# Performance work log

Hardware: AMD Instinct MI355X
Metric: run time of the kernel (lower is better)

The kernel has to match this reference:

```python
import jax, jax.numpy as jnp
import numpy as np

NUM_NODES = 100000
EMBED_DIM = 64
NUM_EDGES = 1250000
NUM_LAYERS = 3


def setup_inputs() -> dict:
    key = jax.random.key(0)
    k1, k2 = jax.random.split(key)
    edge_index = jax.random.randint(k1, (2, NUM_EDGES), 0, NUM_NODES, dtype=jnp.int32)
    # nn.init.normal_(std=0.1)
    emb = 0.1 * jax.random.normal(k2, (NUM_NODES, EMBED_DIM), dtype=jnp.float32)
    return {"edge_index": edge_index, "emb": emb}


def reference(edge_index, emb):
    n = emb.shape[0]
    row, col = edge_index[0], edge_index[1]  # row = source j, col = target i
    # degree of target nodes (PyG degree(col, N))
    deg = jax.ops.segment_sum(jnp.ones((row.shape[0],), emb.dtype), col, num_segments=n)
    deg_inv_sqrt = jnp.where(deg > 0, jax.lax.rsqrt(jnp.maximum(deg, 1.0)), 0.0).astype(emb.dtype)
    norm = deg_inv_sqrt[row] * deg_inv_sqrt[col]  # [E]

    x = emb
    acc = emb  # running sum over layer embeddings (layer 0 included)
    for _ in range(NUM_LAYERS):
        # gather-scale-scatter: out[i] = sum_{(j->i)} norm * x[j]
        msgs = norm[:, None] * x[row]                       # [E, d]
        x = jax.ops.segment_sum(msgs, col, num_segments=n)  # [N, d]
        acc = acc + x
    return acc / (NUM_LAYERS + 1)
```

## Files before the change

kernel.cpp:

```cpp
#include <hip/hip_runtime.h>


#define BKT_SHIFT 7
#define BKT_NODES 128
#define BKT_CAP   2560
#define EPB       2048

__device__ __forceinline__ float lo2f(unsigned u) { return __uint_as_float(u << 16); }
__device__ __forceinline__ float hi2f(unsigned u) { return __uint_as_float(u & 0xFFFF0000u); }
__device__ __forceinline__ unsigned cvt_pk_bf16(float lo, float hi) {
  unsigned r;
  asm("v_cvt_pk_bf16_f32 %0, %1, %2" : "=v"(r) : "v"(lo), "v"(hi));
  return r;
}

__device__ __forceinline__ int wave_scan_incl(int v, int lane) {
#pragma unroll
  for (int off = 1; off < 64; off <<= 1) {
    int t = __shfl_up(v, off, 64);
    if (lane >= off) v += t;
  }
  return v;
}

__global__ void k_init(int* __restrict__ bcursor, int nbkt,
                       unsigned* __restrict__ z0, unsigned* __restrict__ z1,
                       unsigned* __restrict__ z2, int n) {
  int i = blockIdx.x * blockDim.x + threadIdx.x;
  if (i < nbkt) bcursor[i] = i * BKT_CAP;
  if (blockIdx.x == 0 && threadIdx.x < 32) {
    size_t o = (size_t)n * 32 + threadIdx.x;
    z0[o] = 0u; z1[o] = 0u; z2[o] = 0u;
  }
}

__global__ __launch_bounds__(256)
void k_bin(const int* __restrict__ row, const int* __restrict__ col,
           int* __restrict__ bcursor, int* __restrict__ tmp, int E, int nbkt) {
  __shared__ int h[1024];
  int e0 = blockIdx.x * EPB;
  int e1 = min(e0 + EPB, E);
  for (int i = threadIdx.x; i < nbkt; i += 256) h[i] = 0;
  __syncthreads();
  for (int e = e0 + threadIdx.x; e < e1; e += 256)
    atomicAdd(&h[col[e] >> BKT_SHIFT], 1);
  __syncthreads();
  for (int i = threadIdx.x; i < nbkt; i += 256) {
    int c = h[i];
    h[i] = c ? atomicAdd(&bcursor[i], c) : 0;
  }
  __syncthreads();
  for (int e = e0 + threadIdx.x; e < e1; e += 256) {
    int c = col[e], r = row[e];
    int p = atomicAdd(&h[c >> BKT_SHIFT], 1);
    tmp[p] = r | ((c & (BKT_NODES - 1)) << 20);
  }
}

__global__ __launch_bounds__(256)
void k_sort(const int* __restrict__ bcursor, const int* __restrict__ tmp,
            int* __restrict__ srcs, int* __restrict__ obeg, int* __restrict__ oend,
            float* __restrict__ invdeg, float* __restrict__ sdeg,
            const float* __restrict__ emb, unsigned short* __restrict__ z0, int n) {
  __shared__ int hist[BKT_NODES];
  __shared__ int excl[BKT_NODES];
  __shared__ int cur[BKT_NODES];
  __shared__ float sdis[BKT_NODES];
  int b = blockIdx.x;
  int base = b * BKT_CAP;
  int cnt = bcursor[b] - base;
  if (threadIdx.x < BKT_NODES) hist[threadIdx.x] = 0;
  __syncthreads();
  for (int q = threadIdx.x; q < cnt; q += 256)
    atomicAdd(&hist[(unsigned)tmp[base + q] >> 20], 1);
  __syncthreads();
  if (threadIdx.x < 64) {
    int l = threadIdx.x;
    int h0 = hist[2 * l], h1 = hist[2 * l + 1];
    int p0 = (h0 + 3) & ~3, p1 = (h1 + 3) & ~3;
    int v = p0 + p1;
    int incl = wave_scan_incl(v, l);
    int ex = incl - v;
    excl[2 * l] = ex;      excl[2 * l + 1] = ex + p0;
    cur[2 * l] = ex;       cur[2 * l + 1] = ex + p0;
  }
  __syncthreads();
  int node0 = b << BKT_SHIFT;
  if (threadIdx.x < BKT_NODES) {
    int node = node0 + threadIdx.x;
    if (node < n) {
      int d = hist[threadIdx.x];
      int dpad = (d + 3) & ~3;
      int bg = base + excl[threadIdx.x];
      obeg[node] = bg;
      oend[node] = bg + dpad;
      float fd = (float)d;
      invdeg[node] = d ? 1.0f / fd : 0.0f;
      sdeg[node] = sqrtf(fd);
      sdis[threadIdx.x] = d ? rsqrtf(fd) : 0.0f;
      for (int p = d; p < dpad; ++p) srcs[bg + p] = n;
    } else {
      sdis[threadIdx.x] = 0.0f;
    }
  }
  __syncthreads();
  for (int q = threadIdx.x; q < cnt; q += 256) {
    int rec = tmp[base + q];
    int lc = (unsigned)rec >> 20;
    int p = atomicAdd(&cur[lc], 1);
    srcs[base + p] = rec & 0xFFFFF;
  }
  int nloc = min(BKT_NODES, n - node0);
  for (int t = threadIdx.x; t < nloc * 8; t += 256) {
    int rr = t >> 3, q = t & 7;
    float ds = sdis[rr];
    float4 v0 = reinterpret_cast<const float4*>(emb)[(size_t)(node0 + rr) * 16 + 2 * q];
    float4 v1 = reinterpret_cast<const float4*>(emb)[(size_t)(node0 + rr) * 16 + 2 * q + 1];
    uint4 o;
    o.x = cvt_pk_bf16(v0.x * ds, v0.y * ds);
    o.y = cvt_pk_bf16(v0.z * ds, v0.w * ds);
    o.z = cvt_pk_bf16(v1.x * ds, v1.y * ds);
    o.w = cvt_pk_bf16(v1.z * ds, v1.w * ds);
    reinterpret_cast<uint4*>(z0)[(size_t)(node0 + rr) * 8 + q] = o;
  }
}

template <bool FINAL>
__global__ __launch_bounds__(256)
void k_prop(const int* __restrict__ obeg, const int* __restrict__ oend,
            const int* __restrict__ srcs, const unsigned short* __restrict__ z,
            unsigned short* __restrict__ zout, const float* __restrict__ invdeg,
            const float* __restrict__ emb, const unsigned short* __restrict__ z1,
            const unsigned short* __restrict__ z2, const float* __restrict__ sdeg,
            float* __restrict__ out, int n) {
  int lane = threadIdx.x & 63;
  int wid = (blockIdx.x * blockDim.x + threadIdx.x) >> 6;
  int g = lane >> 3, l = lane & 7;
  int node = wid * 8 + g;
  if (node >= n) return;
  const uint4* zv = reinterpret_cast<const uint4*>(z);
  const int4* sv = reinterpret_cast<const int4*>(srcs);

  int kq = obeg[node] >> 2;
  int endq = oend[node] >> 2;

  float s0 = 0.f, s1 = 0.f, s2 = 0.f, s3 = 0.f;
  float s4 = 0.f, s5 = 0.f, s6 = 0.f, s7 = 0.f;

  int4 sq = make_int4(0, 0, 0, 0);
  if (kq < endq) sq = sv[kq];
  while (kq < endq) {
    uint4 a = zv[(size_t)sq.x * 8 + l];
    uint4 b = zv[(size_t)sq.y * 8 + l];
    uint4 c = zv[(size_t)sq.z * 8 + l];
    uint4 d = zv[(size_t)sq.w * 8 + l];
    ++kq;
    sq = sv[(kq < endq) ? kq : (kq - 1)];
    s0 += lo2f(a.x); s1 += hi2f(a.x); s2 += lo2f(a.y); s3 += hi2f(a.y);
    s4 += lo2f(a.z); s5 += hi2f(a.z); s6 += lo2f(a.w); s7 += hi2f(a.w);
    s0 += lo2f(b.x); s1 += hi2f(b.x); s2 += lo2f(b.y); s3 += hi2f(b.y);
    s4 += lo2f(b.z); s5 += hi2f(b.z); s6 += lo2f(b.w); s7 += hi2f(b.w);
    s0 += lo2f(c.x); s1 += hi2f(c.x); s2 += lo2f(c.y); s3 += hi2f(c.y);
    s4 += lo2f(c.z); s5 += hi2f(c.z); s6 += lo2f(c.w); s7 += hi2f(c.w);
    s0 += lo2f(d.x); s1 += hi2f(d.x); s2 += lo2f(d.y); s3 += hi2f(d.y);
    s4 += lo2f(d.z); s5 += hi2f(d.z); s6 += lo2f(d.w); s7 += hi2f(d.w);
  }

  float idg = invdeg[node];
  size_t gi = (size_t)node * 8 + l;
  if (!FINAL) {
    uint4 o;
    o.x = cvt_pk_bf16(s0 * idg, s1 * idg);
    o.y = cvt_pk_bf16(s2 * idg, s3 * idg);
    o.z = cvt_pk_bf16(s4 * idg, s5 * idg);
    o.w = cvt_pk_bf16(s6 * idg, s7 * idg);
    reinterpret_cast<uint4*>(zout)[gi] = o;
  } else {
    float sd = sdeg[node];
    float c = sd * idg;
    uint4 a1 = reinterpret_cast<const uint4*>(z1)[gi];
    uint4 a2 = reinterpret_cast<const uint4*>(z2)[gi];
    float4 e0 = reinterpret_cast<const float4*>(emb)[(size_t)node * 16 + 2 * l];
    float4 e1 = reinterpret_cast<const float4*>(emb)[(size_t)node * 16 + 2 * l + 1];
    float4 o0, o1;
    o0.x = 0.25f * (e0.x + sd * (lo2f(a1.x) + lo2f(a2.x)) + c * s0);
    o0.y = 0.25f * (e0.y + sd * (hi2f(a1.x) + hi2f(a2.x)) + c * s1);
    o0.z = 0.25f * (e0.z + sd * (lo2f(a1.y) + lo2f(a2.y)) + c * s2);
    o0.w = 0.25f * (e0.w + sd * (hi2f(a1.y) + hi2f(a2.y)) + c * s3);
    o1.x = 0.25f * (e1.x + sd * (lo2f(a1.z) + lo2f(a2.z)) + c * s4);
    o1.y = 0.25f * (e1.y + sd * (hi2f(a1.z) + hi2f(a2.z)) + c * s5);
    o1.z = 0.25f * (e1.w + sd * (lo2f(a1.w) + lo2f(a2.w)) + c * s6);
    o1.w = 0.25f * (e1.w + sd * (hi2f(a1.w) + hi2f(a2.w)) + c * s7);
    o1.z = 0.25f * (e1.z + sd * (lo2f(a1.w) + lo2f(a2.w)) + c * s6);
    reinterpret_cast<float4*>(out)[(size_t)node * 16 + 2 * l] = o0;
    reinterpret_cast<float4*>(out)[(size_t)node * 16 + 2 * l + 1] = o1;
  }
}

extern "C" void kernel_launch(void* const* d_in, const int* in_sizes, int n_in,
                              void* d_out, int out_size, void* d_ws, size_t ws_size,
                              hipStream_t stream) {
  const int* edge = (const int*)d_in[0];
  const float* emb = (const float*)d_in[1];
  float* out = (float*)d_out;

  const int E = in_sizes[0] / 2;
  const int n = in_sizes[1] / 64;
  const int* row = edge;
  const int* col = edge + E;
  const int NBKT = (n + BKT_NODES - 1) / BKT_NODES;

  char* ws = (char*)d_ws;
  size_t off = 0;
  auto alloc = [&](size_t bytes) -> void* {
    void* p = ws + off;
    off += (bytes + 255) & ~(size_t)255;
    return p;
  };
  int*   bcursor = (int*)  alloc((size_t)NBKT * 4);
  int*   tmp     = (int*)  alloc((size_t)NBKT * BKT_CAP * 4);
  int*   srcs    = (int*)  alloc((size_t)NBKT * BKT_CAP * 4);
  int*   obeg    = (int*)  alloc((size_t)n * 4);
  int*   oend    = (int*)  alloc((size_t)n * 4);
  float* invdeg  = (float*)alloc((size_t)n * 4);
  float* sdeg    = (float*)alloc((size_t)n * 4);
  unsigned short* z0 = (unsigned short*)alloc((size_t)(n + 1) * 64 * 2);
  unsigned short* z1 = (unsigned short*)alloc((size_t)(n + 1) * 64 * 2);
  unsigned short* z2 = (unsigned short*)alloc((size_t)(n + 1) * 64 * 2);
  (void)ws_size; (void)n_in; (void)out_size;

  const int NBB = (E + EPB - 1) / EPB;
  k_init<<<(NBKT + 255) / 256, 256, 0, stream>>>(bcursor, NBKT,
      (unsigned*)z0, (unsigned*)z1, (unsigned*)z2, n);
  k_bin<<<NBB, 256, 0, stream>>>(row, col, bcursor, tmp, E, NBKT);
  k_sort<<<NBKT, 256, 0, stream>>>(bcursor, tmp, srcs, obeg, oend,
                                   invdeg, sdeg, emb, z0, n);

  const int pg = (n + 31) / 32;
  k_prop<false><<<pg, 256, 0, stream>>>(obeg, oend, srcs, z0, z1, invdeg,
                                        nullptr, nullptr, nullptr, nullptr, nullptr, n);
  k_prop<false><<<pg, 256, 0, stream>>>(obeg, oend, srcs, z1, z2, invdeg,
                                        nullptr, nullptr, nullptr, nullptr, nullptr, n);
  k_prop<true ><<<pg, 256, 0, stream>>>(obeg, oend, srcs, z2, nullptr, invdeg,
                                        emb, z1, z2, sdeg, out, n);
}
```

Baseline: 129.0 us.

## Fuse sort and three propagation layers into one cooperative persistent kernel

Replaces the separate k_sort and three k_prop launches with a single cooperative kernel that loops over buckets and then node groups in grid-stride fashion, separated by grid-wide barriers. The aim is to remove kernel launch gaps and tail drain between the four dependent stages. In exchange it caps occupancy at the cooperative grid size, adds grid.sync cost, and makes host-side occupancy queries on every call. A fallback keeps the old multi-kernel path if the cooperative launch fails.

Result: slower. 475.3 us (+268.6%).

```diff
diff --git a/kernel.cpp b/kernel.cpp
--- a/kernel.cpp
+++ b/kernel.cpp
@@ -1,4 +1,7 @@
 #include <hip/hip_runtime.h>
+#include <hip/hip_cooperative_groups.h>
+
+namespace cg = cooperative_groups;
 
 
 #define BKT_SHIFT 7
@@ -57,16 +60,13 @@
   }
 }
 
-__global__ __launch_bounds__(256)
-void k_sort(const int* __restrict__ bcursor, const int* __restrict__ tmp,
-            int* __restrict__ srcs, int* __restrict__ obeg, int* __restrict__ oend,
-            float* __restrict__ invdeg, float* __restrict__ sdeg,
-            const float* __restrict__ emb, unsigned short* __restrict__ z0, int n) {
-  __shared__ int hist[BKT_NODES];
-  __shared__ int excl[BKT_NODES];
-  __shared__ int cur[BKT_NODES];
-  __shared__ float sdis[BKT_NODES];
-  int b = blockIdx.x;
+
+__device__ __forceinline__ void sort_bucket(
+    int b, const int* __restrict__ bcursor, const int* __restrict__ tmp,
+    int* __restrict__ srcs, int* __restrict__ obeg, int* __restrict__ oend,
+    float* __restrict__ invdeg, float* __restrict__ sdeg,
+    const float* __restrict__ emb, unsigned short* __restrict__ z0, int n,
+    int* hist, int* excl, int* cur, float* sdis) {
   int base = b * BKT_CAP;
   int cnt = bcursor[b] - base;
   if (threadIdx.x < BKT_NODES) hist[threadIdx.x] = 0;
@@ -125,6 +125,92 @@
   }
 }
 
+__device__ __forceinline__ void prop_phase(
+    int wv, int nwaves, int g, int l, int n,
+    const int* __restrict__ obeg, const int* __restrict__ oend,
+    const int* __restrict__ srcs,
+    const unsigned short* __restrict__ z, unsigned short* __restrict__ zout,
+    const float* __restrict__ invdeg, bool final_,
+    const float* __restrict__ emb, const unsigned short* __restrict__ z1,
+    const unsigned short* __restrict__ z2, const float* __restrict__ sdeg,
+    float* __restrict__ out) {
+  const uint4* zv = reinterpret_cast<const uint4*>(z);
+  const int4* sv = reinterpret_cast<const int4*>(srcs);
+  int nwq = (n + 7) >> 3;
+  for (int w = wv; w < nwq; w += nwaves) {
+    int node = w * 8 + g;
+    if (node >= n) continue;
+
+    int kq = obeg[node] >> 2;
+    int endq = oend[node] >> 2;
+
+    float s0 = 0.f, s1 = 0.f, s2 = 0.f, s3 = 0.f;
+    float s4 = 0.f, s5 = 0.f, s6 = 0.f, s7 = 0.f;
+
+    int4 sq = make_int4(0, 0, 0, 0);
+    if (kq < endq) sq = sv[kq];
+    while (kq < endq) {
+      uint4 a = zv[(size_t)sq.x * 8 + l];
+      uint4 b = zv[(size_t)sq.y * 8 + l];
+      uint4 c = zv[(size_t)sq.z * 8 + l];
+      uint4 d = zv[(size_t)sq.w * 8 + l];
+      ++kq;
+      sq = sv[(kq < endq) ? kq : (kq - 1)];
+      s0 += lo2f(a.x); s1 += hi2f(a.x); s2 += lo2f(a.y); s3 += hi2f(a.y);
+      s4 += lo2f(a.z); s5 += hi2f(a.z); s6 += lo2f(a.w); s7 += hi2f(a.w);
+      s0 += lo2f(b.x); s1 += hi2f(b.x); s2 += lo2f(b.y); s3 += hi2f(b.y);
+      s4 += lo2f(b.z); s5 += hi2f(b.z); s6 += lo2f(b.w); s7 += hi2f(b.w);
+      s0 += lo2f(c.x); s1 += hi2f(c.x); s2 += lo2f(c.y); s3 += hi2f(c.y);
+      s4 += lo2f(c.z); s5 += hi2f(c.z); s6 += lo2f(c.w); s7 += hi2f(c.w);
+      s0 += lo2f(d.x); s1 += hi2f(d.x); s2 += lo2f(d.y); s3 += hi2f(d.y);
+      s4 += lo2f(d.z); s5 += hi2f(d.z); s6 += lo2f(d.w); s7 += hi2f(d.w);
+    }
+
+    float idg = invdeg[node];
+    size_t gi = (size_t)node * 8 + l;
+    if (!final_) {
+      uint4 o;
+      o.x = cvt_pk_bf16(s0 * idg, s1 * idg);
+      o.y = cvt_pk_bf16(s2 * idg, s3 * idg);
+      o.z = cvt_pk_bf16(s4 * idg, s5 * idg);
+      o.w = cvt_pk_bf16(s6 * idg, s7 * idg);
+      reinterpret_cast<uint4*>(zout)[gi] = o;
+    } else {
+      float sd = sdeg[node];
+      float c = sd * idg;
+      uint4 a1 = reinterpret_cast<const uint4*>(z1)[gi];
+      uint4 a2 = reinterpret_cast<const uint4*>(z2)[gi];
+      float4 e0 = reinterpret_cast<const float4*>(emb)[(size_t)node * 16 + 2 * l];
+      float4 e1 = reinterpret_cast<const float4*>(emb)[(size_t)node * 16 + 2 * l + 1];
+      float4 o0, o1;
+      o0.x = 0.25f * (e0.x + sd * (lo2f(a1.x) + lo2f(a2.x)) + c * s0);
+      o0.y = 0.25f * (e0.y + sd * (hi2f(a1.x) + hi2f(a2.x)) + c * s1);
+      o0.z = 0.25f * (e0.z + sd * (lo2f(a1.y) + lo2f(a2.y)) + c * s2);
+      o0.w = 0.25f * (e0.w + sd * (hi2f(a1.y) + hi2f(a2.y)) + c * s3);
+      o1.x = 0.25f * (e1.x + sd * (lo2f(a1.z) + lo2f(a2.z)) + c * s4);
+      o1.y = 0.25f * (e1.y + sd * (hi2f(a1.z) + hi2f(a2.z)) + c * s5);
+      o1.z = 0.25f * (e1.z + sd * (lo2f(a1.w) + lo2f(a2.w)) + c * s6);
+      o1.w = 0.25f * (e1.w + sd * (hi2f(a1.w) + hi2f(a2.w)) + c * s7);
+      reinterpret_cast<float4*>(out)[(size_t)node * 16 + 2 * l] = o0;
+      reinterpret_cast<float4*>(out)[(size_t)node * 16 + 2 * l + 1] = o1;
+    }
+  }
+}
+
+
+__global__ __launch_bounds__(256)
+void k_sort(const int* __restrict__ bcursor, const int* __restrict__ tmp,
+            int* __restrict__ srcs, int* __restrict__ obeg, int* __restrict__ oend,
+            float* __restrict__ invdeg, float* __restrict__ sdeg,
+            const float* __restrict__ emb, unsigned short* __restrict__ z0, int n) {
+  __shared__ int hist[BKT_NODES];
+  __shared__ int excl[BKT_NODES];
+  __shared__ int cur[BKT_NODES];
+  __shared__ float sdis[BKT_NODES];
+  sort_bucket(blockIdx.x, bcursor, tmp, srcs, obeg, oend, invdeg, sdeg,
+              emb, z0, n, hist, excl, cur, sdis);
+}
+
 template <bool FINAL>
 __global__ __launch_bounds__(256)
 void k_prop(const int* __restrict__ obeg, const int* __restrict__ oend,
@@ -134,67 +220,48 @@
             const unsigned short* __restrict__ z2, const float* __restrict__ sdeg,
             float* __restrict__ out, int n) {
   int lane = threadIdx.x & 63;
-  int wid = (blockIdx.x * blockDim.x + threadIdx.x) >> 6;
   int g = lane >> 3, l = lane & 7;
-  int node = wid * 8 + g;
-  if (node >= n) return;
-  const uint4* zv = reinterpret_cast<const uint4*>(z);
-  const int4* sv = reinterpret_cast<const int4*>(srcs);
-
-  int kq = obeg[node] >> 2;
-  int endq = oend[node] >> 2;
-
-  float s0 = 0.f, s1 = 0.f, s2 = 0.f, s3 = 0.f;
-  float s4 = 0.f, s5 = 0.f, s6 = 0.f, s7 = 0.f;
-
-  int4 sq = make_int4(0, 0, 0, 0);
-  if (kq < endq) sq = sv[kq];
-  while (kq < endq) {
-    uint4 a = zv[(size_t)sq.x * 8 + l];
-    uint4 b = zv[(size_t)sq.y * 8 + l];
-    uint4 c = zv[(size_t)sq.z * 8 + l];
-    uint4 d = zv[(size_t)sq.w * 8 + l];
-    ++kq;
-    sq = sv[(kq < endq) ? kq : (kq - 1)];
-    s0 += lo2f(a.x); s1 += hi2f(a.x); s2 += lo2f(a.y); s3 += hi2f(a.y);
-    s4 += lo2f(a.z); s5 += hi2f(a.z); s6 += lo2f(a.w); s7 += hi2f(a.w);
-    s0 += lo2f(b.x); s1 += hi2f(b.x); s2 += lo2f(b.y); s3 += hi2f(b.y);
-    s4 += lo2f(b.z); s5 += hi2f(b.z); s6 += lo2f(b.w); s7 += hi2f(b.w);
-    s0 += lo2f(c.x); s1 += hi2f(c.x); s2 += lo2f(c.y); s3 += hi2f(c.y);
-    s4 += lo2f(c.z); s5 += hi2f(c.z); s6 += lo2f(c.w); s7 += hi2f(c.w);
-    s0 += lo2f(d.x); s1 += hi2f(d.x); s2 += lo2f(d.y); s3 += hi2f(d.y);
-    s4 += lo2f(d.z); s5 += hi2f(d.z); s6 += lo2f(d.w); s7 += hi2f(d.w);
-  }
-
-  float idg = invdeg[node];
-  size_t gi = (size_t)node * 8 + l;
-  if (!FINAL) {
-    uint4 o;
-    o.x = cvt_pk_bf16(s0 * idg, s1 * idg);
-    o.y = cvt_pk_bf16(s2 * idg, s3 * idg);
-    o.z = cvt_pk_bf16(s4 * idg, s5 * idg);
-    o.w = cvt_pk_bf16(s6 * idg, s7 * idg);
-    reinterpret_cast<uint4*>(zout)[gi] = o;
-  } else {
-    float sd = sdeg[node];
-    float c = sd * idg;
-    uint4 a1 = reinterpret_cast<const uint4*>(z1)[gi];
-    uint4 a2 = reinterpret_cast<const uint4*>(z2)[gi];
-    float4 e0 = reinterpret_cast<const float4*>(emb)[(size_t)node * 16 + 2 * l];
-    float4 e1 = reinterpret_cast<const float4*>(emb)[(size_t)node * 16 + 2 * l + 1];
-    float4 o0, o1;
-    o0.x = 0.25f * (e0.x + sd * (lo2f(a1.x) + lo2f(a2.x)) + c * s0);
-    o0.y = 0.25f * (e0.y + sd * (hi2f(a1.x) + hi2f(a2.x)) + c * s1);
-    o0.z = 0.25f * (e0.z + sd * (lo2f(a1.y) + lo2f(a2.y)) + c * s2);
-    o0.w = 0.25f * (e0.w + sd * (hi2f(a1.y) + hi2f(a2.y)) + c * s3);
-    o1.x = 0.25f * (e1.x + sd * (lo2f(a1.z) + lo2f(a2.z)) + c * s4);
-    o1.y = 0.25f * (e1.y + sd * (hi2f(a1.z) + hi2f(a2.z)) + c * s5);
-    o1.z = 0.25f * (e1.w + sd * (lo2f(a1.w) + lo2f(a2.w)) + c * s6);
-    o1.w = 0.25f * (e1.w + sd * (hi2f(a1.w) + hi2f(a2.w)) + c * s7);
-    o1.z = 0.25f * (e1.z + sd * (lo2f(a1.w) + lo2f(a2.w)) + c * s6);
-    reinterpret_cast<float4*>(out)[(size_t)node * 16 + 2 * l] = o0;
-    reinterpret_cast<float4*>(out)[(size_t)node * 16 + 2 * l + 1] = o1;
-  }
+  int wv = (blockIdx.x * 256 + threadIdx.x) >> 6;
+  int nwaves = gridDim.x * 4;
+  prop_phase(wv, nwaves, g, l, n, obeg, oend, srcs, z, zout, invdeg,
+             FINAL, emb, z1, z2, sdeg, out);
+}
+
+__global__ __launch_bounds__(256, 4)
+void k_coop(const int* __restrict__ bcursor, const int* __restrict__ tmp,
+            int* __restrict__ srcs, int* __restrict__ obeg, int* __restrict__ oend,
+            float* __restrict__ invdeg, float* __restrict__ sdeg,
+            const float* __restrict__ emb, unsigned short* __restrict__ z0,
+            unsigned short* __restrict__ z1, unsigned short* __restrict__ z2,
+            float* __restrict__ out, int n, int nbkt) {
+  cg::grid_group grid = cg::this_grid();
+
+  {
+    __shared__ int hist[BKT_NODES];
+    __shared__ int excl[BKT_NODES];
+    __shared__ int cur[BKT_NODES];
+    __shared__ float sdis[BKT_NODES];
+    for (int b = blockIdx.x; b < nbkt; b += gridDim.x) {
+      sort_bucket(b, bcursor, tmp, srcs, obeg, oend, invdeg, sdeg,
+                  emb, z0, n, hist, excl, cur, sdis);
+      __syncthreads();
+    }
+  }
+  grid.sync();
+
+  int lane = threadIdx.x & 63;
+  int g = lane >> 3, l = lane & 7;
+  int wv = (blockIdx.x * 256 + threadIdx.x) >> 6;
+  int nwaves = gridDim.x * 4;
+
+  prop_phase(wv, nwaves, g, l, n, obeg, oend, srcs, z0, z1, invdeg,
+             false, nullptr, nullptr, nullptr, nullptr, nullptr);
+  grid.sync();
+  prop_phase(wv, nwaves, g, l, n, obeg, oend, srcs, z1, z2, invdeg,
+             false, nullptr, nullptr, nullptr, nullptr, nullptr);
+  grid.sync();
+  prop_phase(wv, nwaves, g, l, n, obeg, oend, srcs, z2, nullptr, invdeg,
+             true, emb, z1, z2, sdeg, out);
 }
 
 extern "C" void kernel_launch(void* const* d_in, const int* in_sizes, int n_in,
@@ -233,14 +300,36 @@
   k_init<<<(NBKT + 255) / 256, 256, 0, stream>>>(bcursor, NBKT,
       (unsigned*)z0, (unsigned*)z1, (unsigned*)z2, n);
   k_bin<<<NBB, 256, 0, stream>>>(row, col, bcursor, tmp, E, NBKT);
-  k_sort<<<NBKT, 256, 0, stream>>>(bcursor, tmp, srcs, obeg, oend,
-                                   invdeg, sdeg, emb, z0, n);
-
-  const int pg = (n + 31) / 32;
-  k_prop<false><<<pg, 256, 0, stream>>>(obeg, oend, srcs, z0, z1, invdeg,
-                                        nullptr, nullptr, nullptr, nullptr, nullptr, n);
-  k_prop<false><<<pg, 256, 0, stream>>>(obeg, oend, srcs, z1, z2, invdeg,
-                                        nullptr, nullptr, nullptr, nullptr, nullptr, n);
-  k_prop<true ><<<pg, 256, 0, stream>>>(obeg, oend, srcs, z2, nullptr, invdeg,
-                                        emb, z1, z2, sdeg, out, n);
-}
+
+  bool coop_ok = false;
+  int maxBlocksPerCU = 0, nCU = 0, dev = 0;
+  if (hipGetDevice(&dev) == hipSuccess &&
+      hipDeviceGetAttribute(&nCU, hipDeviceAttributeMultiprocessorCount, dev) == hipSuccess &&
+      hipOccupancyMaxActiveBlocksPerMultiprocessor(&maxBlocksPerCU,
+          (const void*)k_coop, 256, 0) == hipSuccess &&
+      maxBlocksPerCU > 0 && nCU > 0) {
+    int grid = maxBlocksPerCU * nCU;
+    int maxUseful = (n + 31) / 32;
+    if (grid > maxUseful) grid = maxUseful;
+    int n_ = n, nbkt_ = NBKT;
+    void* cargs[] = {
+      (void*)&bcursor, (void*)&tmp, (void*)&srcs, (void*)&obeg, (void*)&oend,
+      (void*)&invdeg, (void*)&sdeg, (void*)&emb, (void*)&z0, (void*)&z1,
+      (void*)&z2, (void*)&out, (void*)&n_, (void*)&nbkt_
+    };
+    coop_ok = (hipLaunchCooperativeKernel((const void*)k_coop, dim3(grid),
+                                          dim3(256), cargs, 0, stream) == hipSuccess);
+  }
+
+  if (!coop_ok) {
+    k_sort<<<NBKT, 256, 0, stream>>>(bcursor, tmp, srcs, obeg, oend,
+                                     invdeg, sdeg, emb, z0, n);
+    const int pg = (n + 31) / 32;
+    k_prop<false><<<pg, 256, 0, stream>>>(obeg, oend, srcs, z0, z1, invdeg,
+                                          nullptr, nullptr, nullptr, nullptr, nullptr, n);
+    k_prop<false><<<pg, 256, 0, stream>>>(obeg, oend, srcs, z1, z2, invdeg,
+                                          nullptr, nullptr, nullptr, nullptr, nullptr, n);
+    k_prop<true ><<<pg, 256, 0, stream>>>(obeg, oend, srcs, z2, nullptr, invdeg,
+                                          emb, z1, z2, sdeg, out, n);
+  }
+}
```
